# Kernel optimization log

Hardware: AMD Instinct MI355X
Metric: run time of the kernel (lower is better)

## Reference

```python
import jax, jax.numpy as jnp
import numpy as np

NUM_HEADS = 12
HEAD_DIM = 64  # d_out // num_heads = 768 // 12


def setup_inputs() -> dict:
    key = jax.random.key(0)
    ks = jax.random.split(key, 6)
    b, s, d = 2, 2048, 768
    x = jax.random.normal(ks[0], (b, s, d), dtype=jnp.float32)
    sc = 1.0 / np.sqrt(d)
    Wq = jax.random.normal(ks[1], (d, d), dtype=jnp.float32) * sc
    Wk = jax.random.normal(ks[2], (d, d), dtype=jnp.float32) * sc
    Wv = jax.random.normal(ks[3], (d, d), dtype=jnp.float32) * sc
    Wo = jax.random.normal(ks[4], (d, d), dtype=jnp.float32) * sc
    bo = jnp.zeros((d,), dtype=jnp.float32)
    return {"x": x, "Wq": Wq, "Wk": Wk, "Wv": Wv, "Wo": Wo, "bo": bo}


def reference(x, Wq, Wk, Wv, Wo, bo):
    # Prefill from a fresh sliding-window KV cache: cache == new K/V,
    # standard causal (triu) mask. dropout=0 (eval).
    b, s, d = x.shape
    H, Dh = NUM_HEADS, HEAD_DIM

    def proj(W):  # torch Linear: x @ W^T, then split heads -> [b, H, s, Dh]
        return (x @ W.T).reshape(b, s, H, Dh).transpose(0, 2, 1, 3)

    q, k, v = proj(Wq), proj(Wk), proj(Wv)

    scores = jnp.einsum('bhqd,bhkd->bhqk', q, k)          # [b,H,s,s]
    causal = jnp.triu(jnp.ones((s, s), dtype=bool), k=1)  # future positions
    scores = jnp.where(causal[None, None], -jnp.inf, scores)
    attn = jax.nn.softmax(scores / np.sqrt(Dh), axis=-1)

    ctx = jnp.einsum('bhqk,bhkd->bhqd', attn, v)          # [b,H,s,Dh]
    ctx = ctx.transpose(0, 2, 1, 3).reshape(b, s, d)      # [b,s,d_out]
    return ctx @ Wo.T + bo
```

## Files before the change

### kernel.cpp

```cpp
#include <hip/hip_runtime.h>
#include <stdint.h>

typedef __attribute__((ext_vector_type(4))) float f32x4;
typedef __attribute__((ext_vector_type(8))) short s16x8;

#if __has_builtin(__builtin_amdgcn_exp2f)
#define EXP2(x) __builtin_amdgcn_exp2f(x)
#else
#define EXP2(x) exp2f(x)
#endif

#define GL2LDS(g, s)                                                        \
  __builtin_amdgcn_global_load_lds(                                         \
      (const __attribute__((address_space(1))) void*)(g),                   \
      (__attribute__((address_space(3))) void*)(s), 16, 0, 0)

__device__ __forceinline__ unsigned short tobf(float x) {
  uint32_t u = __builtin_bit_cast(uint32_t, x);
  u += 0x7fffu + ((u >> 16) & 1u);
  return (unsigned short)(u >> 16);
}

__device__ __forceinline__ uint32_t pk2(float lo, float hi) {
  return (uint32_t)tobf(lo) | ((uint32_t)tobf(hi) << 16);
}

__device__ __forceinline__ uint32_t pktrunc(float lo, float hi) {
  return __builtin_amdgcn_perm(__builtin_bit_cast(uint32_t, hi),
                               __builtin_bit_cast(uint32_t, lo), 0x07060302u);
}

__global__ __launch_bounds__(256) void cvt_all(
    const float* __restrict__ x,  const float* __restrict__ wq,
    const float* __restrict__ wk, const float* __restrict__ wv,
    const float* __restrict__ wo, unsigned short* __restrict__ outb) {
  int i = blockIdx.x * 256 + threadIdx.x;
  if (i >= 1376256) return;
  const float* in;
  int j;
  if (i < 786432) { in = x; j = i; }
  else {
    int k = i - 786432;
    int sel = k / 147456;
    j = k - sel * 147456;
    in = (sel == 0) ? wq : (sel == 1) ? wk : (sel == 2) ? wv : wo;
  }
  float4 v = reinterpret_cast<const float4*>(in)[j];
  uint2 o; o.x = pk2(v.x, v.y); o.y = pk2(v.z, v.w);
  reinterpret_cast<uint2*>(outb)[i] = o;
}

__global__ __launch_bounds__(512) void qkv_gemm(
    const unsigned short* __restrict__ xb,
    const unsigned short* __restrict__ wq,
    const unsigned short* __restrict__ wk,
    const unsigned short* __restrict__ wv,
    unsigned short* __restrict__ q_ws,
    unsigned short* __restrict__ k_ws,
    unsigned short* __restrict__ vt_ws) {
  __shared__ unsigned short As[2][4096];
  __shared__ unsigned short Bs[2][4096];
  const int t = threadIdx.x;
  const int l = t & 63, w = t >> 6;
  const int wm = w >> 2, wn = w & 3;
  const int lr = l & 15, lg = l >> 4;

  const int id = (int)blockIdx.x;
  const int xcd = id & 7;
  const int g = id >> 3;
  const int nt = g % 18;
  const int tileM = ((g / 18) * 8 + xcd) * 128;
  const int wsel = nt / 6;
  const unsigned short* W = (wsel == 0) ? wq : ((wsel == 1) ? wk : wv);
  const int tileN = (nt % 6) * 128;

  const int srow = w * 16 + (l >> 2);
  const int scol = (((l & 3) ^ ((l >> 2) & 3))) * 8;

#define QSTAGE(buf, k0_)                                                       \
  do {                                                                         \
    GL2LDS(&xb[(tileM + srow) * 768 + (k0_) + scol], &As[buf][w * 512]);       \
    GL2LDS(&W [(tileN + srow) * 768 + (k0_) + scol], &Bs[buf][w * 512]);       \
  } while (0)

  const int chf = ((lg ^ (lr & 3)) << 3);

  f32x4 acc[4][2];
  const f32x4 z4 = {0.f, 0.f, 0.f, 0.f};
#pragma unroll
  for (int i = 0; i < 4; ++i)
#pragma unroll
    for (int j = 0; j < 2; ++j) acc[i][j] = z4;

  QSTAGE(0, 0);
  QSTAGE(1, 32);
  for (int it = 0; it < 24; ++it) {
    const int c = it & 1;
    if (it < 23) {
      asm volatile("s_waitcnt vmcnt(2)" ::: "memory");
    } else {
      asm volatile("s_waitcnt vmcnt(0)" ::: "memory");
    }
    __builtin_amdgcn_s_barrier();
    __builtin_amdgcn_sched_barrier(0);

    s16x8 a[4], b[2];
#pragma unroll
    for (int mi = 0; mi < 4; ++mi)
      a[mi] = *(const s16x8*)&As[c][(wm * 64 + mi * 16 + lr) * 32 + chf];
#pragma unroll
    for (int ni = 0; ni < 2; ++ni)
      b[ni] = *(const s16x8*)&Bs[c][(wn * 32 + ni * 16 + lr) * 32 + chf];
    __builtin_amdgcn_s_setprio(1);
#pragma unroll
    for (int mi = 0; mi < 4; ++mi)
#pragma unroll
      for (int ni = 0; ni < 2; ++ni)
        acc[mi][ni] = __builtin_amdgcn_mfma_f32_16x16x32_bf16(a[mi], b[ni], acc[mi][ni], 0, 0, 0);
    __builtin_amdgcn_s_setprio(0);

    if (it < 22) {
      asm volatile("s_waitcnt lgkmcnt(0)" ::: "memory");
      __builtin_amdgcn_s_barrier();
      QSTAGE(c, (it + 2) * 32);
    }
  }
#undef QSTAGE

#pragma unroll
  for (int mi = 0; mi < 4; ++mi)
#pragma unroll
    for (int ni = 0; ni < 2; ++ni) {
      int m0 = tileM + wm * 64 + mi * 16 + lg * 4;
      int n = tileN + wn * 32 + ni * 16 + lr;
      int bb = m0 >> 11, sq0 = m0 & 2047;
      int h = n >> 6, dh = n & 63;
      if (wsel == 0) {
#pragma unroll
        for (int r = 0; r < 4; ++r)
          q_ws[((bb * 12 + h) * 2048 + sq0 + r) * 64 + dh] =
              tobf(acc[mi][ni][r] * 0.18033688011112042f);
      } else if (wsel == 1) {
#pragma unroll
        for (int r = 0; r < 4; ++r)
          k_ws[((bb * 12 + h) * 2048 + sq0 + r) * 64 + dh] = tobf(acc[mi][ni][r]);
      } else {
        uint2 o;
        o.x = pk2(acc[mi][ni][0], acc[mi][ni][1]);
        o.y = pk2(acc[mi][ni][2], acc[mi][ni][3]);
        *(uint2*)&vt_ws[((bb * 12 + h) * 64 + dh) * 2048 + sq0] = o;
      }
    }
}

__global__ __launch_bounds__(128) void attn_kernel(
    const unsigned short* __restrict__ q_ws,
    const unsigned short* __restrict__ k_ws,
    const unsigned short* __restrict__ vt_ws,
    unsigned short* __restrict__ ctx) {
  __shared__ unsigned short Ks[2][4096];
  __shared__ unsigned short Vs[2][4096];

  const int t = threadIdx.x;
  const int l = t & 63, w = t >> 6;
  const int lr = l & 15, lg = l >> 4;

  const int id = (int)blockIdx.x;
  const int xcd = id & 7;
  const int g = id >> 3;
  const int qt = 63 - g / 3;
  const int bh = (g % 3) * 8 + xcd;

  const int rb = w * 8 + (l >> 3);
  const int gcol = ((l & 7) ^ (l >> 3)) * 8;
  const int krow = 8 * ((rb >> 2) & 3) + (rb & 3);
  const unsigned short* kgp  = &k_ws[(bh * 2048 + krow) * 64 + gcol];
  const unsigned short* vbase = &vt_ws[(bh * 64 + rb) * 2048 + gcol];

#define STAGE(buf, kt_)                                                \
  do {                                                                 \
    GL2LDS(kgp + (kt_) * 4096,           &Ks[buf][w * 512]);           \
    GL2LDS(kgp + (kt_) * 4096 + 2048,    &Ks[buf][1024 + w * 512]);    \
    GL2LDS(kgp + (kt_) * 4096 + 256,     &Ks[buf][2048 + w * 512]);    \
    GL2LDS(kgp + (kt_) * 4096 + 2304,    &Ks[buf][3072 + w * 512]);    \
    GL2LDS(vbase + (kt_) * 64,           &Vs[buf][w * 512]);           \
    GL2LDS(vbase + (kt_) * 64 + 32768,   &Vs[buf][1024 + w * 512]);    \
    GL2LDS(vbase + (kt_) * 64 + 65536,   &Vs[buf][2048 + w * 512]);    \
    GL2LDS(vbase + (kt_) * 64 + 98304,   &Vs[buf][3072 + w * 512]);    \
  } while (0)

  const int cks0 = (lg * 8) ^ ((lr & 7) << 3);
  const int cks1 = (32 + lg * 8) ^ ((lr & 7) << 3);

  const int bb = bh / 12, hh = bh % 12;
  const f32x4 z4 = {0.f, 0.f, 0.f, 0.f};

  const int ktmax = qt >> 1;
  const int qg = qt * 32 + w * 16 + lr;

  s16x8 qa[2];
#pragma unroll
  for (int kk = 0; kk < 2; ++kk)
    qa[kk] = *(const s16x8*)&q_ws[(bh * 2048 + qg) * 64 + kk * 32 + lg * 8];

  f32x4 o[4];
#pragma unroll
  for (int di = 0; di < 4; ++di) o[di] = z4;
  float lrun = 0.f;
  f32x4 s[4];

  STAGE(0, 0);
  __syncthreads();

  __builtin_amdgcn_s_setprio(1);
#pragma unroll
  for (int ni = 0; ni < 4; ++ni) {
    s16x8 kb0 = *(const s16x8*)&Ks[0][ni * 1024 + lr * 64 + cks0];
    s16x8 kb1 = *(const s16x8*)&Ks[0][ni * 1024 + lr * 64 + cks1];
    s[ni] = __builtin_amdgcn_mfma_f32_16x16x32_bf16(kb0, qa[0], z4, 0, 0, 0);
    s[ni] = __builtin_amdgcn_mfma_f32_16x16x32_bf16(kb1, qa[1], s[ni], 0, 0, 0);
  }
  __builtin_amdgcn_s_setprio(0);
  if (ktmax >= 1) STAGE(1, 1);

  int c = 0;
  for (int kt = 0; kt <= ktmax; ++kt) {
    if (kt == ktmax) {
#pragma unroll
      for (int ni = 0; ni < 4; ++ni)
#pragma unroll
        for (int r = 0; r < 4; ++r) {
          int kg_ = kt * 64 + ((ni & 1) << 5) + (lg << 3) + ((ni >> 1) << 2) + r;
          if (kg_ > qg) s[ni][r] = -1e30f;
        }
    }

#pragma unroll
    for (int ni = 0; ni < 4; ++ni)
#pragma unroll
      for (int r = 0; r < 4; ++r) s[ni][r] = EXP2(s[ni][r]);
    {
      float t0 = (s[0][0] + s[0][1]) + (s[0][2] + s[0][3]);
      float t1 = (s[1][0] + s[1][1]) + (s[1][2] + s[1][3]);
      float t2 = (s[2][0] + s[2][1]) + (s[2][2] + s[2][3]);
      float t3 = (s[3][0] + s[3][1]) + (s[3][2] + s[3][3]);
      lrun += (t0 + t1) + (t2 + t3);
    }

    s16x8 pa[2];
#pragma unroll
    for (int kk = 0; kk < 2; ++kk) {
      uint4 u;
      u.x = pktrunc(s[kk][0],     s[kk][1]);
      u.y = pktrunc(s[kk][2],     s[kk][3]);
      u.z = pktrunc(s[kk + 2][0], s[kk + 2][1]);
      u.w = pktrunc(s[kk + 2][2], s[kk + 2][3]);
      pa[kk] = __builtin_bit_cast(s16x8, u);
    }

    const bool have_next = (kt < ktmax);
    __builtin_amdgcn_s_setprio(1);
    if (have_next) {
      __syncthreads();
#pragma unroll
      for (int ni = 0; ni < 4; ++ni) {
        s16x8 kb0 = *(const s16x8*)&Ks[c ^ 1][ni * 1024 + lr * 64 + cks0];
        s16x8 kb1 = *(const s16x8*)&Ks[c ^ 1][ni * 1024 + lr * 64 + cks1];
        s[ni] = __builtin_amdgcn_mfma_f32_16x16x32_bf16(kb0, qa[0], z4, 0, 0, 0);
        s[ni] = __builtin_amdgcn_mfma_f32_16x16x32_bf16(kb1, qa[1], s[ni], 0, 0, 0);
      }
    }
#pragma unroll
    for (int di = 0; di < 4; ++di) {
      s16x8 vb0 = *(const s16x8*)&Vs[c][di * 1024 + lr * 64 + cks0];
      s16x8 vb1 = *(const s16x8*)&Vs[c][di * 1024 + lr * 64 + cks1];
      o[di] = __builtin_amdgcn_mfma_f32_16x16x32_bf16(vb0, pa[0], o[di], 0, 0, 0);
      o[di] = __builtin_amdgcn_mfma_f32_16x16x32_bf16(vb1, pa[1], o[di], 0, 0, 0);
    }
    __builtin_amdgcn_s_setprio(0);

    if (kt + 2 <= ktmax) {
      __syncthreads();
      STAGE(c, kt + 2);
    }
    c ^= 1;
  }

  float lt = lrun + __shfl_xor(lrun, 16);
  lt += __shfl_xor(lt, 32);
  const float rl = 1.0f / lt;
#pragma unroll
  for (int di = 0; di < 4; ++di) {
    uint2 ov;
    ov.x = pk2(o[di][0] * rl, o[di][1] * rl);
    ov.y = pk2(o[di][2] * rl, o[di][3] * rl);
    *(uint2*)&ctx[(bb * 2048 + qg) * 768 + hh * 64 + di * 16 + lg * 4] = ov;
  }
#undef STAGE
}

__global__ __launch_bounds__(64) void out_gemm(
    const unsigned short* __restrict__ ctxb,
    const unsigned short* __restrict__ wo,
    const float* __restrict__ bo,
    float* __restrict__ out) {
  __shared__ unsigned short As[2][2048];
  __shared__ unsigned short Bs[2][2048];
  const int l = threadIdx.x;
  const int lr = l & 15, lg = l >> 4;

  const int id = (int)blockIdx.x;
  const int xcd = id & 7;
  const int g = id >> 3;
  const int tileN = (g % 12) * 64;
  const int tileM = ((g / 12) * 8 + xcd) * 64;

  const int srow = l >> 2;
  const int scol = ((l & 3) ^ (srow & 3)) * 8;

#define OSTAGE(buf, k0_)                                                       \
  do {                                                                         \
    _Pragma("unroll")                                                          \
    for (int i_ = 0; i_ < 4; ++i_) {                                           \
      GL2LDS(&ctxb[(tileM + i_ * 16 + srow) * 768 + (k0_) + scol],             \
             &As[buf][i_ * 512]);                                              \
      GL2LDS(&wo  [(tileN + i_ * 16 + srow) * 768 + (k0_) + scol],             \
             &Bs[buf][i_ * 512]);                                              \
    }                                                                          \
  } while (0)

  const int chf = ((lg ^ (lr & 3)) << 3);

  f32x4 acc[4][4];
  const f32x4 z4 = {0.f, 0.f, 0.f, 0.f};
#pragma unroll
  for (int i = 0; i < 4; ++i)
#pragma unroll
    for (int j = 0; j < 4; ++j) acc[i][j] = z4;

  OSTAGE(0, 0);
  __syncthreads();
  int c = 0;
  for (int it = 0; it < 24; ++it) {
    if (it < 23) OSTAGE(c ^ 1, (it + 1) * 32);
    s16x8 a[4], b[4];
#pragma unroll
    for (int mi = 0; mi < 4; ++mi)
      a[mi] = *(const s16x8*)&As[c][(mi * 16 + lr) * 32 + chf];
#pragma unroll
    for (int ni = 0; ni < 4; ++ni)
      b[ni] = *(const s16x8*)&Bs[c][(ni * 16 + lr) * 32 + chf];
    __builtin_amdgcn_s_setprio(1);
#pragma unroll
    for (int mi = 0; mi < 4; ++mi)
#pragma unroll
      for (int ni = 0; ni < 4; ++ni)
        acc[mi][ni] = __builtin_amdgcn_mfma_f32_16x16x32_bf16(a[mi], b[ni], acc[mi][ni], 0, 0, 0);
    __builtin_amdgcn_s_setprio(0);
    if (it < 23) {
      __syncthreads();
      c ^= 1;
    }
  }
#undef OSTAGE

#pragma unroll
  for (int mi = 0; mi < 4; ++mi)
#pragma unroll
    for (int ni = 0; ni < 4; ++ni)
#pragma unroll
      for (int r = 0; r < 4; ++r) {
        int m = tileM + mi * 16 + lg * 4 + r;
        int n = tileN + ni * 16 + lr;
        out[m * 768 + n] = acc[mi][ni][r] + bo[n];
      }
}

extern "C" void kernel_launch(void* const* d_in, const int* in_sizes, int n_in,
                              void* d_out, int out_size, void* d_ws, size_t ws_size,
                              hipStream_t stream) {
  const float* x  = (const float*)d_in[0];
  const float* Wq = (const float*)d_in[1];
  const float* Wk = (const float*)d_in[2];
  const float* Wv = (const float*)d_in[3];
  const float* Wo = (const float*)d_in[4];
  const float* bo = (const float*)d_in[5];
  float* out = (float*)d_out;

  char* ws = (char*)d_ws;
  unsigned short* xb    = (unsigned short*)(ws);
  unsigned short* wqb   = (unsigned short*)(ws + 6291456);
  unsigned short* wkb   = (unsigned short*)(ws + 7471104);
  unsigned short* wvb   = (unsigned short*)(ws + 8650752);
  unsigned short* wob   = (unsigned short*)(ws + 9830400);
  unsigned short* q_ws  = (unsigned short*)(ws + 11010048);
  unsigned short* k_ws  = (unsigned short*)(ws + 17301504);
  unsigned short* vt_ws = (unsigned short*)(ws + 23592960);
  unsigned short* ctx   = (unsigned short*)(ws + 29884416);

  cvt_all<<<5376, 256, 0, stream>>>(x, Wq, Wk, Wv, Wo, (unsigned short*)ws);
  qkv_gemm<<<576, 512, 0, stream>>>(xb, wqb, wkb, wvb, q_ws, k_ws, vt_ws);
  attn_kernel<<<1536, 128, 0, stream>>>(q_ws, k_ws, vt_ws, ctx);
  out_gemm<<<768, 64, 0, stream>>>(ctx, wob, bo, out);
}
```

Baseline: 82.65 us.

## Process two 32-row query tiles per attention block to reuse K/V tiles

Each attention block now handles a 64-row query tile as two 16-row-per-wave sub-tiles (A and B) that share every staged K/V LDS tile, halving the grid to 768 blocks. This halves K/V global-to-LDS traffic and barrier count per query row and gives each wave twice the independent MFMA work to interleave. In exchange it doubles accumulator register use, which may lower occupancy, and the smaller grid gives the GPU fewer blocks to balance the causal work across.

```diff
diff --git a/kernel.cpp b/kernel.cpp
--- a/kernel.cpp
+++ b/kernel.cpp
@@ -168,7 +168,7 @@
   const int id = (int)blockIdx.x;
   const int xcd = id & 7;
   const int g = id >> 3;
-  const int qt = 63 - g / 3;
+  const int j = 31 - g / 3;
   const int bh = (g % 3) * 8 + xcd;
 
   const int rb = w * 8 + (l >> 3);
@@ -195,19 +195,22 @@
   const int bb = bh / 12, hh = bh % 12;
   const f32x4 z4 = {0.f, 0.f, 0.f, 0.f};
 
-  const int ktmax = qt >> 1;
-  const int qg = qt * 32 + w * 16 + lr;
-
-  s16x8 qa[2];
-#pragma unroll
-  for (int kk = 0; kk < 2; ++kk)
-    qa[kk] = *(const s16x8*)&q_ws[(bh * 2048 + qg) * 64 + kk * 32 + lg * 8];
-
-  f32x4 o[4];
-#pragma unroll
-  for (int di = 0; di < 4; ++di) o[di] = z4;
-  float lrun = 0.f;
-  f32x4 s[4];
+  const int ktmax = j;
+  const int qgA = 64 * j + w * 16 + lr;
+  const int qgB = qgA + 32;
+
+  s16x8 qaA[2], qaB[2];
+#pragma unroll
+  for (int kk = 0; kk < 2; ++kk) {
+    qaA[kk] = *(const s16x8*)&q_ws[(bh * 2048 + qgA) * 64 + kk * 32 + lg * 8];
+    qaB[kk] = *(const s16x8*)&q_ws[(bh * 2048 + qgB) * 64 + kk * 32 + lg * 8];
+  }
+
+  f32x4 oA[4], oB[4];
+#pragma unroll
+  for (int di = 0; di < 4; ++di) { oA[di] = z4; oB[di] = z4; }
+  float lrunA = 0.f, lrunB = 0.f;
+  f32x4 sA[4], sB[4];
 
   STAGE(0, 0);
   __syncthreads();
@@ -217,8 +220,10 @@
   for (int ni = 0; ni < 4; ++ni) {
     s16x8 kb0 = *(const s16x8*)&Ks[0][ni * 1024 + lr * 64 + cks0];
     s16x8 kb1 = *(const s16x8*)&Ks[0][ni * 1024 + lr * 64 + cks1];
-    s[ni] = __builtin_amdgcn_mfma_f32_16x16x32_bf16(kb0, qa[0], z4, 0, 0, 0);
-    s[ni] = __builtin_amdgcn_mfma_f32_16x16x32_bf16(kb1, qa[1], s[ni], 0, 0, 0);
+    sA[ni] = __builtin_amdgcn_mfma_f32_16x16x32_bf16(kb0, qaA[0], z4, 0, 0, 0);
+    sA[ni] = __builtin_amdgcn_mfma_f32_16x16x32_bf16(kb1, qaA[1], sA[ni], 0, 0, 0);
+    sB[ni] = __builtin_amdgcn_mfma_f32_16x16x32_bf16(kb0, qaB[0], z4, 0, 0, 0);
+    sB[ni] = __builtin_amdgcn_mfma_f32_16x16x32_bf16(kb1, qaB[1], sB[ni], 0, 0, 0);
   }
   __builtin_amdgcn_s_setprio(0);
   if (ktmax >= 1) STAGE(1, 1);
@@ -231,31 +236,45 @@
 #pragma unroll
         for (int r = 0; r < 4; ++r) {
           int kg_ = kt * 64 + ((ni & 1) << 5) + (lg << 3) + ((ni >> 1) << 2) + r;
-          if (kg_ > qg) s[ni][r] = -1e30f;
+          if (kg_ > qgA) sA[ni][r] = -1e30f;
+          if (kg_ > qgB) sB[ni][r] = -1e30f;
         }
     }
 
 #pragma unroll
     for (int ni = 0; ni < 4; ++ni)
 #pragma unroll
-      for (int r = 0; r < 4; ++r) s[ni][r] = EXP2(s[ni][r]);
+      for (int r = 0; r < 4; ++r) {
+        sA[ni][r] = EXP2(sA[ni][r]);
+        sB[ni][r] = EXP2(sB[ni][r]);
+      }
     {
-      float t0 = (s[0][0] + s[0][1]) + (s[0][2] + s[0][3]);
-      float t1 = (s[1][0] + s[1][1]) + (s[1][2] + s[1][3]);
-      float t2 = (s[2][0] + s[2][1]) + (s[2][2] + s[2][3]);
-      float t3 = (s[3][0] + s[3][1]) + (s[3][2] + s[3][3]);
-      lrun += (t0 + t1) + (t2 + t3);
-    }
-
-    s16x8 pa[2];
+      float a0 = (sA[0][0] + sA[0][1]) + (sA[0][2] + sA[0][3]);
+      float a1 = (sA[1][0] + sA[1][1]) + (sA[1][2] + sA[1][3]);
+      float a2 = (sA[2][0] + sA[2][1]) + (sA[2][2] + sA[2][3]);
+      float a3 = (sA[3][0] + sA[3][1]) + (sA[3][2] + sA[3][3]);
+      lrunA += (a0 + a1) + (a2 + a3);
+      float b0 = (sB[0][0] + sB[0][1]) + (sB[0][2] + sB[0][3]);
+      float b1 = (sB[1][0] + sB[1][1]) + (sB[1][2] + sB[1][3]);
+      float b2 = (sB[2][0] + sB[2][1]) + (sB[2][2] + sB[2][3]);
+      float b3 = (sB[3][0] + sB[3][1]) + (sB[3][2] + sB[3][3]);
+      lrunB += (b0 + b1) + (b2 + b3);
+    }
+
+    s16x8 paA[2], paB[2];
 #pragma unroll
     for (int kk = 0; kk < 2; ++kk) {
-      uint4 u;
-      u.x = pktrunc(s[kk][0],     s[kk][1]);
-      u.y = pktrunc(s[kk][2],     s[kk][3]);
-      u.z = pktrunc(s[kk + 2][0], s[kk + 2][1]);
-      u.w = pktrunc(s[kk + 2][2], s[kk + 2][3]);
-      pa[kk] = __builtin_bit_cast(s16x8, u);
+      uint4 ua, ub;
+      ua.x = pktrunc(sA[kk][0],     sA[kk][1]);
+      ua.y = pktrunc(sA[kk][2],     sA[kk][3]);
+      ua.z = pktrunc(sA[kk + 2][0], sA[kk + 2][1]);
+      ua.w = pktrunc(sA[kk + 2][2], sA[kk + 2][3]);
+      paA[kk] = __builtin_bit_cast(s16x8, ua);
+      ub.x = pktrunc(sB[kk][0],     sB[kk][1]);
+      ub.y = pktrunc(sB[kk][2],     sB[kk][3]);
+      ub.z = pktrunc(sB[kk + 2][0], sB[kk + 2][1]);
+      ub.w = pktrunc(sB[kk + 2][2], sB[kk + 2][3]);
+      paB[kk] = __builtin_bit_cast(s16x8, ub);
     }
 
     const bool have_next = (kt < ktmax);
@@ -266,16 +285,20 @@
       for (int ni = 0; ni < 4; ++ni) {
         s16x8 kb0 = *(const s16x8*)&Ks[c ^ 1][ni * 1024 + lr * 64 + cks0];
         s16x8 kb1 = *(const s16x8*)&Ks[c ^ 1][ni * 1024 + lr * 64 + cks1];
-        s[ni] = __builtin_amdgcn_mfma_f32_16x16x32_bf16(kb0, qa[0], z4, 0, 0, 0);
-        s[ni] = __builtin_amdgcn_mfma_f32_16x16x32_bf16(kb1, qa[1], s[ni], 0, 0, 0);
+        sA[ni] = __builtin_amdgcn_mfma_f32_16x16x32_bf16(kb0, qaA[0], z4, 0, 0, 0);
+        sA[ni] = __builtin_amdgcn_mfma_f32_16x16x32_bf16(kb1, qaA[1], sA[ni], 0, 0, 0);
+        sB[ni] = __builtin_amdgcn_mfma_f32_16x16x32_bf16(kb0, qaB[0], z4, 0, 0, 0);
+        sB[ni] = __builtin_amdgcn_mfma_f32_16x16x32_bf16(kb1, qaB[1], sB[ni], 0, 0, 0);
       }
     }
 #pragma unroll
     for (int di = 0; di < 4; ++di) {
       s16x8 vb0 = *(const s16x8*)&Vs[c][di * 1024 + lr * 64 + cks0];
       s16x8 vb1 = *(const s16x8*)&Vs[c][di * 1024 + lr * 64 + cks1];
-      o[di] = __builtin_amdgcn_mfma_f32_16x16x32_bf16(vb0, pa[0], o[di], 0, 0, 0);
-      o[di] = __builtin_amdgcn_mfma_f32_16x16x32_bf16(vb1, pa[1], o[di], 0, 0, 0);
+      oA[di] = __builtin_amdgcn_mfma_f32_16x16x32_bf16(vb0, paA[0], oA[di], 0, 0, 0);
+      oA[di] = __builtin_amdgcn_mfma_f32_16x16x32_bf16(vb1, paA[1], oA[di], 0, 0, 0);
+      oB[di] = __builtin_amdgcn_mfma_f32_16x16x32_bf16(vb0, paB[0], oB[di], 0, 0, 0);
+      oB[di] = __builtin_amdgcn_mfma_f32_16x16x32_bf16(vb1, paB[1], oB[di], 0, 0, 0);
     }
     __builtin_amdgcn_s_setprio(0);
 
@@ -286,15 +309,21 @@
     c ^= 1;
   }
 
-  float lt = lrun + __shfl_xor(lrun, 16);
-  lt += __shfl_xor(lt, 32);
-  const float rl = 1.0f / lt;
+  float ltA = lrunA + __shfl_xor(lrunA, 16);
+  ltA += __shfl_xor(ltA, 32);
+  float ltB = lrunB + __shfl_xor(lrunB, 16);
+  ltB += __shfl_xor(ltB, 32);
+  const float rlA = 1.0f / ltA;
+  const float rlB = 1.0f / ltB;
 #pragma unroll
   for (int di = 0; di < 4; ++di) {
-    uint2 ov;
-    ov.x = pk2(o[di][0] * rl, o[di][1] * rl);
-    ov.y = pk2(o[di][2] * rl, o[di][3] * rl);
-    *(uint2*)&ctx[(bb * 2048 + qg) * 768 + hh * 64 + di * 16 + lg * 4] = ov;
+    uint2 oa, ob;
+    oa.x = pk2(oA[di][0] * rlA, oA[di][1] * rlA);
+    oa.y = pk2(oA[di][2] * rlA, oA[di][3] * rlA);
+    *(uint2*)&ctx[(bb * 2048 + qgA) * 768 + hh * 64 + di * 16 + lg * 4] = oa;
+    ob.x = pk2(oB[di][0] * rlB, oB[di][1] * rlB);
+    ob.y = pk2(oB[di][2] * rlB, oB[di][3] * rlB);
+    *(uint2*)&ctx[(bb * 2048 + qgB) * 768 + hh * 64 + di * 16 + lg * 4] = ob;
   }
 #undef STAGE
 }
@@ -400,6 +429,6 @@
 
   cvt_all<<<5376, 256, 0, stream>>>(x, Wq, Wk, Wv, Wo, (unsigned short*)ws);
   qkv_gemm<<<576, 512, 0, stream>>>(xb, wqb, wkb, wvb, q_ws, k_ws, vt_ws);
-  attn_kernel<<<1536, 128, 0, stream>>>(q_ws, k_ws, vt_ws, ctx);
+  attn_kernel<<<768, 128, 0, stream>>>(q_ws, k_ws, vt_ws, ctx);
   out_gemm<<<768, 64, 0, stream>>>(ctx, wob, bo, out);
 }
```

Result: slower. 87.99 us (+6.5%).
